# Optimization experiments

Measured on AMD Instinct MI355X. Metric: run time of the kernel, lower is better.

Reference implementation:

```python
import jax, jax.numpy as jnp
import numpy as np

N, E, G = 50000, 800000, 64        # nodes, edges, graphs in batch
IN, HID, OUT = 64, 128, 8


def gcn_conv(x, W, b, src, dst, num_nodes):
    """GCNConv: h = D^-1/2 (A+I) D^-1/2 (x W) + b, self-loops already in src/dst."""
    h = x @ W                                              # [N, out]
    deg = jax.ops.segment_sum(jnp.ones_like(dst, dtype=h.dtype), dst,
                              num_segments=num_nodes)      # [N]
    dinv = jax.lax.rsqrt(jnp.maximum(deg, 1.0))
    norm = dinv[src] * dinv[dst]                           # [E+N]
    msg = h[src] * norm[:, None]                           # gather + scale
    out = jax.ops.segment_sum(msg, dst, num_segments=num_nodes)
    return out + b


def global_mean_pool(x, batch, num_graphs):
    s = jax.ops.segment_sum(x, batch, num_segments=num_graphs)
    cnt = jax.ops.segment_sum(jnp.ones((x.shape[0],), x.dtype), batch,
                              num_segments=num_graphs)
    return s / jnp.maximum(cnt, 1.0)[:, None]


def setup_inputs() -> dict:
    key = jax.random.key(0)
    ks = jax.random.split(key, 11)
    def glorot(k, fi, fo):
        return jax.random.normal(k, (fi, fo), jnp.float32) * np.float32(1.0 / np.sqrt(fi))
    return {
        "x": jax.random.normal(ks[0], (N, IN), jnp.float32),
        "W1": glorot(ks[1], IN, HID),  "b1": jnp.zeros((HID,), jnp.float32),
        "W2": glorot(ks[2], HID, HID), "b2": jnp.zeros((HID,), jnp.float32),
        "W3": glorot(ks[3], HID, HID), "b3": jnp.zeros((HID,), jnp.float32),
        "Wh": glorot(ks[4], HID, OUT), "bh": jnp.zeros((OUT,), jnp.float32),
        "edge_index": jax.random.randint(ks[5], (2, E), 0, N),
        "batch": jnp.sort(jax.random.randint(ks[6], (N,), 0, G)),
    }


def reference(x, W1, b1, W2, b2, W3, b3, Wh, bh, edge_index, batch):
    loops = jnp.arange(N, dtype=edge_index.dtype)
    src = jnp.concatenate([edge_index[0], loops])          # add self-loops
    dst = jnp.concatenate([edge_index[1], loops])
    h = jax.nn.relu(gcn_conv(x, W1, b1, src, dst, N))
    h = jax.nn.relu(gcn_conv(h, W2, b2, src, dst, N))
    h = gcn_conv(h, W3, b3, src, dst, N)
    g = global_mean_pool(h, batch, G)                      # [G, HID]
    return g @ Wh + bh                                     # [G, OUT]
```

## Files before the change

### kernel.cpp

```cpp
#include <hip/hip_runtime.h>

typedef short bf8_t __attribute__((ext_vector_type(8)));
typedef float f32x4 __attribute__((ext_vector_type(4)));

__device__ inline unsigned short f2bf(float f) {
    unsigned u = __float_as_uint(f);
    return (unsigned short)((u + 0x7fff + ((u >> 16) & 1)) >> 16);
}


__global__ void deg_kernel(const int* __restrict__ dst, int* __restrict__ deg,
                           int* __restrict__ rank, int E) {
    int e = blockIdx.x * 256 + threadIdx.x;
    if (e < E) rank[e] = atomicAdd(&deg[dst[e]], 1);
}

__global__ void scan_blocksum(const int* __restrict__ deg, int* __restrict__ bsum,
                              float* __restrict__ dinv, int n) {
    int i = blockIdx.x * 256 + threadIdx.x;
    int d = (i < n) ? (deg[i] + 1) : 0;
    if (i < n) dinv[i] = rsqrtf((float)d);
    int v = d;
    for (int off = 32; off > 0; off >>= 1) v += __shfl_down(v, off, 64);
    __shared__ int ws[4];
    if ((threadIdx.x & 63) == 0) ws[threadIdx.x >> 6] = v;
    __syncthreads();
    if (threadIdx.x == 0) bsum[blockIdx.x] = ws[0] + ws[1] + ws[2] + ws[3];
}

__global__ void scan_offsets(const int* __restrict__ bsum, int* __restrict__ boff, int nblk) {
    __shared__ int buf[256];
    int tid = threadIdx.x;
    int v = (tid < nblk) ? bsum[tid] : 0;
    buf[tid] = v;
    __syncthreads();
    for (int off = 1; off < 256; off <<= 1) {
        int t = (tid >= off) ? buf[tid - off] : 0;
        __syncthreads();
        buf[tid] += t;
        __syncthreads();
    }
    if (tid < nblk) boff[tid] = buf[tid] - v;
}

__global__ void scan_rowptr(const int* __restrict__ deg, const int* __restrict__ boff,
                            int* __restrict__ row_ptr, int n) {
    __shared__ int buf[256];
    int tid = threadIdx.x;
    int i = blockIdx.x * 256 + tid;
    int v = (i < n) ? (deg[i] + 1) : 0;
    buf[tid] = v;
    __syncthreads();
    for (int off = 1; off < 256; off <<= 1) {
        int t = (tid >= off) ? buf[tid - off] : 0;
        __syncthreads();
        buf[tid] += t;
        __syncthreads();
    }
    int excl = buf[tid] - v + boff[blockIdx.x];
    if (i < n) row_ptr[i] = excl;
    if (i == n - 1) row_ptr[n] = excl + v;
}

__global__ void fill_kernel(const int* __restrict__ src, const int* __restrict__ dst,
                            const int* __restrict__ rank,
                            const int* __restrict__ row_ptr,
                            int* __restrict__ csr_src, int E, int n) {
    int e = blockIdx.x * 256 + threadIdx.x;
    if (e < E) {
        int s = src[e], d = dst[e];
        int pos = row_ptr[d] + 1 + rank[e];
        __builtin_nontemporal_store(s, &csr_src[pos]);
    } else if (e < E + n) {
        int s = e - E;
        __builtin_nontemporal_store(s, &csr_src[row_ptr[s]]);
    }
}

__global__ void x2bf_kernel(const float* __restrict__ x, const float* __restrict__ dinv,
                            unsigned* __restrict__ x16, int total8) {
    int i = blockIdx.x * 256 + threadIdx.x;
    if (i >= total8) return;
    float dn = dinv[i >> 3];
    const float4* x4 = (const float4*)x;
    float4 a = x4[i * 2], b = x4[i * 2 + 1];
    uint4 o;
    o.x = (unsigned)f2bf(a.x * dn) | ((unsigned)f2bf(a.y * dn) << 16);
    o.y = (unsigned)f2bf(a.z * dn) | ((unsigned)f2bf(a.w * dn) << 16);
    o.z = (unsigned)f2bf(b.x * dn) | ((unsigned)f2bf(b.y * dn) << 16);
    o.w = (unsigned)f2bf(b.z * dn) | ((unsigned)f2bf(b.w * dn) << 16);
    ((uint4*)x16)[i] = o;
}

__global__ void wt_all(const float* __restrict__ W1, const float* __restrict__ W2,
                       const float* __restrict__ W3,
                       unsigned short* __restrict__ Wt1, unsigned short* __restrict__ Wt2,
                       unsigned short* __restrict__ Wt3) {
    int i = blockIdx.x * 256 + threadIdx.x;
    if (i < 8192) {
        int nn = i / 64, k = i - nn * 64;
        Wt1[i] = f2bf(W1[k * 128 + nn]);
    } else if (i < 24576) {
        int j = i - 8192;
        int nn = j / 128, k = j - nn * 128;
        Wt2[j] = f2bf(W2[k * 128 + nn]);
    } else if (i < 40960) {
        int j = i - 24576;
        int nn = j / 128, k = j - nn * 128;
        Wt3[j] = f2bf(W3[k * 128 + nn]);
    }
}


__device__ inline void bf8_add(uint4 a, float* acc) {
#pragma unroll
    for (int j = 0; j < 4; ++j) {
        unsigned u = ((const unsigned*)&a)[j];
        acc[2 * j]     += __uint_as_float(u << 16);
        acc[2 * j + 1] += __uint_as_float(u & 0xffff0000u);
    }
}

__device__ inline uint4 pack_bf8(const float* v, float dn) {
    uint4 o;
    o.x = (unsigned)f2bf(v[0] * dn) | ((unsigned)f2bf(v[1] * dn) << 16);
    o.y = (unsigned)f2bf(v[2] * dn) | ((unsigned)f2bf(v[3] * dn) << 16);
    o.z = (unsigned)f2bf(v[4] * dn) | ((unsigned)f2bf(v[5] * dn) << 16);
    o.w = (unsigned)f2bf(v[6] * dn) | ((unsigned)f2bf(v[7] * dn) << 16);
    return o;
}

template<int K, bool RELU, bool BF16OUT>
__global__ __launch_bounds__(256) void agg_gemm(
        const unsigned short* __restrict__ in, const unsigned short* __restrict__ Wt16,
        const float* __restrict__ bias, void* __restrict__ outp,
        const int* __restrict__ row_ptr, const int* __restrict__ csr_src,
        const float* __restrict__ dinv, int n) {
    constexpr int KS = K / 32;
    __shared__ unsigned short As[16 * K];
    int w = threadIdx.x >> 6, lane = threadIdx.x & 63;
    int base = blockIdx.x * 16;
    int lr = lane & 15, lk = lane >> 4;

    bf8_t B[2][KS];
#pragma unroll
    for (int f = 0; f < 2; ++f) {
        int col = w * 32 + f * 16 + lr;
#pragma unroll
        for (int ks = 0; ks < KS; ++ks)
            B[f][ks] = *reinterpret_cast<const bf8_t*>(&Wt16[(size_t)col * K + ks * 32 + lk * 8]);
    }

    const uint4* in4 = (const uint4*)in;
    int g = lane >> 4;
    int row = w * 4 + g;
    int node = base + row;
    float acc[8] = {0.f, 0.f, 0.f, 0.f, 0.f, 0.f, 0.f, 0.f};

    if (K == 128) {
        int col = lane & 15;
        if (node < n) {
            int beg = row_ptr[node], end = row_ptr[node + 1];
            int i = beg;
            for (; i + 1 < end; i += 2) {
                int s0 = csr_src[i], s1 = csr_src[i + 1];
                uint4 a = in4[(size_t)s0 * 16 + col];
                uint4 b = in4[(size_t)s1 * 16 + col];
                bf8_add(a, acc);
                bf8_add(b, acc);
            }
            if (i < end) bf8_add(in4[(size_t)csr_src[i] * 16 + col], acc);
        }
        float dn = (node < n) ? dinv[node] : 0.f;
        int off = row * K + ((col * 8) ^ ((row & 7) << 3));
        *(uint4*)&As[off] = pack_bf8(acc, dn);
    } else {
        int sub = (lane >> 3) & 1;
        int col = lane & 7;
        if (node < n) {
            int beg = row_ptr[node], end = row_ptr[node + 1];
            int i = beg + sub;
            for (; i + 2 < end; i += 4) {
                int s0 = csr_src[i], s1 = csr_src[i + 2];
                uint4 a = in4[(size_t)s0 * 8 + col];
                uint4 b = in4[(size_t)s1 * 8 + col];
                bf8_add(a, acc);
                bf8_add(b, acc);
            }
            if (i < end) bf8_add(in4[(size_t)csr_src[i] * 8 + col], acc);
        }
#pragma unroll
        for (int j = 0; j < 8; ++j)
            acc[j] += __shfl_xor(acc[j], 8, 64);
        if (sub == 0) {
            float dn = (node < n) ? dinv[node] : 0.f;
            int off = row * K + ((col * 8) ^ ((row & 7) << 3));
            *(uint4*)&As[off] = pack_bf8(acc, dn);
        }
    }
    __syncthreads();

    f32x4 pacc[2] = {};
#pragma unroll
    for (int ks = 0; ks < KS; ++ks) {
        int off = lr * K + (((ks * 32) + lk * 8) ^ ((lr & 7) << 3));
        bf8_t a = *reinterpret_cast<const bf8_t*>(&As[off]);
#pragma unroll
        for (int f = 0; f < 2; ++f)
            pacc[f] = __builtin_amdgcn_mfma_f32_16x16x32_bf16(B[f][ks], a, pacc[f], 0, 0, 0);
    }

    int orow = base + lr;
    if (orow < n) {
        float dnx = BF16OUT ? dinv[orow] : 1.f;
#pragma unroll
        for (int f = 0; f < 2; ++f) {
            int c0 = w * 32 + f * 16 + lk * 4;
            float4 bv = *(const float4*)&bias[c0];
            float v0 = pacc[f][0] + bv.x, v1 = pacc[f][1] + bv.y;
            float v2 = pacc[f][2] + bv.z, v3 = pacc[f][3] + bv.w;
            if (RELU) {
                v0 = fmaxf(v0, 0.f); v1 = fmaxf(v1, 0.f);
                v2 = fmaxf(v2, 0.f); v3 = fmaxf(v3, 0.f);
            }
            if (BF16OUT) {
                uint2 o;
                o.x = (unsigned)f2bf(v0 * dnx) | ((unsigned)f2bf(v1 * dnx) << 16);
                o.y = (unsigned)f2bf(v2 * dnx) | ((unsigned)f2bf(v3 * dnx) << 16);
                *(uint2*)&((unsigned short*)outp)[(size_t)orow * 128 + c0] = o;
            } else {
                *(float4*)&((float*)outp)[(size_t)orow * 128 + c0] = make_float4(v0, v1, v2, v3);
            }
        }
    }
}


__global__ void gstart_bs(const int* __restrict__ batch, int* __restrict__ gstart,
                          int n, int G) {
    int g = blockIdx.x * blockDim.x + threadIdx.x;
    if (g > G) return;
    int lo = 0, hi = n;
    while (lo < hi) {
        int mid = (lo + hi) >> 1;
        if (batch[mid] < g) lo = mid + 1; else hi = mid;
    }
    gstart[g] = lo;
}

#define PSPLIT 16
__global__ __launch_bounds__(256) void pool_part(
        const float* __restrict__ h, const int* __restrict__ gstart,
        float* __restrict__ part) {
    int g = blockIdx.x >> 4, sp = blockIdx.x & (PSPLIT - 1);
    int tid = threadIdx.x;
    int c = tid & 127, rs = tid >> 7;
    int beg = gstart[g], end = gstart[g + 1];
    int len = end - beg;
    int chunk = (len + PSPLIT - 1) >> 4;
    int r0 = beg + sp * chunk;
    int r1 = min(r0 + chunk, end);
    float acc = 0.f;
    for (int r = r0 + rs; r < r1; r += 2)
        acc += h[(size_t)r * 128 + c];
    __shared__ float buf[256];
    buf[tid] = acc;
    __syncthreads();
    if (rs == 0)
        part[(size_t)blockIdx.x * 128 + c] = buf[c] + buf[c + 128];
}

__global__ __launch_bounds__(128) void pool_final(
        const float* __restrict__ part, const int* __restrict__ gstart,
        float* __restrict__ gout) {
    int g = blockIdx.x;
    int c = threadIdx.x;
    float acc = 0.f;
#pragma unroll
    for (int sp = 0; sp < PSPLIT; ++sp)
        acc += part[((size_t)g * PSPLIT + sp) * 128 + c];
    int cnt = gstart[g + 1] - gstart[g];
    gout[g * 128 + c] = acc / fmaxf((float)cnt, 1.f);
}

__global__ void head_kernel(const float* __restrict__ g, const float* __restrict__ Wh,
                            const float* __restrict__ bh, float* __restrict__ out, int G) {
    int tid = blockIdx.x * blockDim.x + threadIdx.x;
    if (tid >= G * 8) return;
    int gi = tid >> 3, o = tid & 7;
    float acc = bh[o];
    for (int k = 0; k < 128; ++k)
        acc = fmaf(g[gi * 128 + k], Wh[k * 8 + o], acc);
    out[tid] = acc;
}


extern "C" void kernel_launch(void* const* d_in, const int* in_sizes, int n_in,
                              void* d_out, int out_size, void* d_ws, size_t ws_size,
                              hipStream_t stream) {
    const float* x  = (const float*)d_in[0];
    const float* W1 = (const float*)d_in[1];
    const float* b1 = (const float*)d_in[2];
    const float* W2 = (const float*)d_in[3];
    const float* b2 = (const float*)d_in[4];
    const float* W3 = (const float*)d_in[5];
    const float* b3 = (const float*)d_in[6];
    const float* Wh = (const float*)d_in[7];
    const float* bh = (const float*)d_in[8];
    const int* edge_index = (const int*)d_in[9];
    const int* batch = (const int*)d_in[10];
    (void)n_in; (void)ws_size;

    const int N = in_sizes[10];
    const int E = in_sizes[9] / 2;
    const int G = out_size / 8;
    const int* esrc = edge_index;
    const int* edst = edge_index + E;

    size_t off = 0;
    auto take = [&](size_t bytes) {
        void* p = (char*)d_ws + off;
        off += (bytes + 255) & ~(size_t)255;
        return p;
    };
    int*   deg      = (int*)take((size_t)N * 4);
    float* dinv     = (float*)take((size_t)N * 4);
    int*   row_ptr  = (int*)take((size_t)(N + 1) * 4);
    int*   rank     = (int*)take((size_t)E * 4);
    int*   csr_src  = (int*)take((size_t)(E + N) * 4);
    int*   bsum     = (int*)take(256 * 4);
    int*   boff     = (int*)take(256 * 4);
    int*   gstart   = (int*)take((size_t)(G + 1) * 4);
    float* part     = (float*)take((size_t)G * PSPLIT * 128 * 4);
    float* gpool    = (float*)take((size_t)G * 128 * 4);
    unsigned short* x16  = (unsigned short*)take((size_t)N * 64 * 2);
    unsigned short* h16a = (unsigned short*)take((size_t)N * 128 * 2);
    unsigned short* h16b = (unsigned short*)take((size_t)N * 128 * 2);
    unsigned short* Wt1  = (unsigned short*)take((size_t)128 * 64 * 2);
    unsigned short* Wt2  = (unsigned short*)take((size_t)128 * 128 * 2);
    unsigned short* Wt3  = (unsigned short*)take((size_t)128 * 128 * 2);
    float* bufA     = (float*)take((size_t)N * 128 * 4);

    int nblk = (N + 255) / 256;
    int fgrid = (N + 15) / 16;

    hipMemsetAsync(deg, 0, (size_t)N * 4, stream);

    deg_kernel<<<(E + 255) / 256, 256, 0, stream>>>(edst, deg, rank, E);
    scan_blocksum<<<nblk, 256, 0, stream>>>(deg, bsum, dinv, N);
    scan_offsets<<<1, 256, 0, stream>>>(bsum, boff, nblk);
    scan_rowptr<<<nblk, 256, 0, stream>>>(deg, boff, row_ptr, N);
    fill_kernel<<<(E + N + 255) / 256, 256, 0, stream>>>(esrc, edst, rank, row_ptr, csr_src, E, N);
    x2bf_kernel<<<(N * 64 / 8 + 255) / 256, 256, 0, stream>>>(x, dinv, (unsigned*)x16, N * 64 / 8);
    wt_all<<<(40960 + 255) / 256, 256, 0, stream>>>(W1, W2, W3, Wt1, Wt2, Wt3);

    agg_gemm<64,  true,  true ><<<fgrid, 256, 0, stream>>>(x16,  Wt1, b1, h16a, row_ptr, csr_src, dinv, N);
    agg_gemm<128, true,  true ><<<fgrid, 256, 0, stream>>>(h16a, Wt2, b2, h16b, row_ptr, csr_src, dinv, N);
    agg_gemm<128, false, false><<<fgrid, 256, 0, stream>>>(h16b, Wt3, b3, bufA, row_ptr, csr_src, dinv, N);

    gstart_bs<<<1, 256, 0, stream>>>(batch, gstart, N, G);
    pool_part<<<G * PSPLIT, 256, 0, stream>>>(bufA, gstart, part);
    pool_final<<<G, 128, 0, stream>>>(part, gstart, gpool);
    head_kernel<<<(G * 8 + 255) / 256, 256, 0, stream>>>(gpool, Wh, bh, (float*)d_out, G);
}
```

Measured before the change: 226.9 us.

## Store CSR indices and ranks as 16-bit, prefetch neighbor indices, fuse gstart search

Narrows the per-edge rank and CSR source-index arrays from 32-bit to 16-bit, halving the bytes written in the fill step and read by each of the three aggregation kernels. The gather loops now software-prefetch the next pair of neighbor indices, and the CSR buffer is padded so those reads stay in bounds. The separate gstart binary-search kernel is removed, and the pooling kernels compute graph bounds inline, saving one launch. The 16-bit indices cannot represent node ids up to N=50000 that exceed 32767 as signed, though they fit as unsigned. Per-node degrees above 65535 would overflow the rank field.

```diff
diff --git a/kernel.cpp b/kernel.cpp
--- a/kernel.cpp
+++ b/kernel.cpp
@@ -2,17 +2,18 @@
 
 typedef short bf8_t __attribute__((ext_vector_type(8)));
 typedef float f32x4 __attribute__((ext_vector_type(4)));
-
-__device__ inline unsigned short f2bf(float f) {
+typedef unsigned short u16;
+
+__device__ inline u16 f2bf(float f) {
     unsigned u = __float_as_uint(f);
-    return (unsigned short)((u + 0x7fff + ((u >> 16) & 1)) >> 16);
+    return (u16)((u + 0x7fff + ((u >> 16) & 1)) >> 16);
 }
 
 
 __global__ void deg_kernel(const int* __restrict__ dst, int* __restrict__ deg,
-                           int* __restrict__ rank, int E) {
+                           u16* __restrict__ rank, int E) {
     int e = blockIdx.x * 256 + threadIdx.x;
-    if (e < E) rank[e] = atomicAdd(&deg[dst[e]], 1);
+    if (e < E) rank[e] = (u16)atomicAdd(&deg[dst[e]], 1);
 }
 
 __global__ void scan_blocksum(const int* __restrict__ deg, int* __restrict__ bsum,
@@ -63,17 +64,17 @@
 }
 
 __global__ void fill_kernel(const int* __restrict__ src, const int* __restrict__ dst,
-                            const int* __restrict__ rank,
+                            const u16* __restrict__ rank,
                             const int* __restrict__ row_ptr,
-                            int* __restrict__ csr_src, int E, int n) {
+                            u16* __restrict__ csr_src, int E, int n) {
     int e = blockIdx.x * 256 + threadIdx.x;
     if (e < E) {
         int s = src[e], d = dst[e];
-        int pos = row_ptr[d] + 1 + rank[e];
-        __builtin_nontemporal_store(s, &csr_src[pos]);
+        int pos = row_ptr[d] + 1 + (int)rank[e];
+        __builtin_nontemporal_store((u16)s, &csr_src[pos]);
     } else if (e < E + n) {
         int s = e - E;
-        __builtin_nontemporal_store(s, &csr_src[row_ptr[s]]);
+        __builtin_nontemporal_store((u16)s, &csr_src[row_ptr[s]]);
     }
 }
 
@@ -94,8 +95,8 @@
 
 __global__ void wt_all(const float* __restrict__ W1, const float* __restrict__ W2,
                        const float* __restrict__ W3,
-                       unsigned short* __restrict__ Wt1, unsigned short* __restrict__ Wt2,
-                       unsigned short* __restrict__ Wt3) {
+                       u16* __restrict__ Wt1, u16* __restrict__ Wt2,
+                       u16* __restrict__ Wt3) {
     int i = blockIdx.x * 256 + threadIdx.x;
     if (i < 8192) {
         int nn = i / 64, k = i - nn * 64;
@@ -132,12 +133,12 @@
 
 template<int K, bool RELU, bool BF16OUT>
 __global__ __launch_bounds__(256) void agg_gemm(
-        const unsigned short* __restrict__ in, const unsigned short* __restrict__ Wt16,
+        const u16* __restrict__ in, const u16* __restrict__ Wt16,
         const float* __restrict__ bias, void* __restrict__ outp,
-        const int* __restrict__ row_ptr, const int* __restrict__ csr_src,
+        const int* __restrict__ row_ptr, const u16* __restrict__ csr_src,
         const float* __restrict__ dinv, int n) {
     constexpr int KS = K / 32;
-    __shared__ unsigned short As[16 * K];
+    __shared__ u16 As[16 * K];
     int w = threadIdx.x >> 6, lane = threadIdx.x & 63;
     int base = blockIdx.x * 16;
     int lr = lane & 15, lk = lane >> 4;
@@ -162,14 +163,16 @@
         if (node < n) {
             int beg = row_ptr[node], end = row_ptr[node + 1];
             int i = beg;
+            int s0 = csr_src[i], s1 = csr_src[i + 1];
             for (; i + 1 < end; i += 2) {
-                int s0 = csr_src[i], s1 = csr_src[i + 1];
+                int t0 = csr_src[i + 2], t1 = csr_src[i + 3];
                 uint4 a = in4[(size_t)s0 * 16 + col];
                 uint4 b = in4[(size_t)s1 * 16 + col];
                 bf8_add(a, acc);
                 bf8_add(b, acc);
+                s0 = t0; s1 = t1;
             }
-            if (i < end) bf8_add(in4[(size_t)csr_src[i] * 16 + col], acc);
+            if (i < end) bf8_add(in4[(size_t)s0 * 16 + col], acc);
         }
         float dn = (node < n) ? dinv[node] : 0.f;
         int off = row * K + ((col * 8) ^ ((row & 7) << 3));
@@ -180,14 +183,16 @@
         if (node < n) {
             int beg = row_ptr[node], end = row_ptr[node + 1];
             int i = beg + sub;
+            int s0 = csr_src[i], s1 = csr_src[i + 2];
             for (; i + 2 < end; i += 4) {
-                int s0 = csr_src[i], s1 = csr_src[i + 2];
+                int t0 = csr_src[i + 4], t1 = csr_src[i + 6];
                 uint4 a = in4[(size_t)s0 * 8 + col];
                 uint4 b = in4[(size_t)s1 * 8 + col];
                 bf8_add(a, acc);
                 bf8_add(b, acc);
+                s0 = t0; s1 = t1;
             }
-            if (i < end) bf8_add(in4[(size_t)csr_src[i] * 8 + col], acc);
+            if (i < end) bf8_add(in4[(size_t)s0 * 8 + col], acc);
         }
 #pragma unroll
         for (int j = 0; j < 8; ++j)
@@ -227,7 +232,7 @@
                 uint2 o;
                 o.x = (unsigned)f2bf(v0 * dnx) | ((unsigned)f2bf(v1 * dnx) << 16);
                 o.y = (unsigned)f2bf(v2 * dnx) | ((unsigned)f2bf(v3 * dnx) << 16);
-                *(uint2*)&((unsigned short*)outp)[(size_t)orow * 128 + c0] = o;
+                *(uint2*)&((u16*)outp)[(size_t)orow * 128 + c0] = o;
             } else {
                 *(float4*)&((float*)outp)[(size_t)orow * 128 + c0] = make_float4(v0, v1, v2, v3);
             }
@@ -236,26 +241,23 @@
 }
 
 
-__global__ void gstart_bs(const int* __restrict__ batch, int* __restrict__ gstart,
-                          int n, int G) {
-    int g = blockIdx.x * blockDim.x + threadIdx.x;
-    if (g > G) return;
+__device__ inline int lbound(const int* __restrict__ batch, int n, int g) {
     int lo = 0, hi = n;
     while (lo < hi) {
         int mid = (lo + hi) >> 1;
         if (batch[mid] < g) lo = mid + 1; else hi = mid;
     }
-    gstart[g] = lo;
+    return lo;
 }
 
 #define PSPLIT 16
 __global__ __launch_bounds__(256) void pool_part(
-        const float* __restrict__ h, const int* __restrict__ gstart,
-        float* __restrict__ part) {
+        const float* __restrict__ h, const int* __restrict__ batch,
+        float* __restrict__ part, int n) {
     int g = blockIdx.x >> 4, sp = blockIdx.x & (PSPLIT - 1);
     int tid = threadIdx.x;
     int c = tid & 127, rs = tid >> 7;
-    int beg = gstart[g], end = gstart[g + 1];
+    int beg = lbound(batch, n, g), end = lbound(batch, n, g + 1);
     int len = end - beg;
     int chunk = (len + PSPLIT - 1) >> 4;
     int r0 = beg + sp * chunk;
@@ -271,15 +273,15 @@
 }
 
 __global__ __launch_bounds__(128) void pool_final(
-        const float* __restrict__ part, const int* __restrict__ gstart,
-        float* __restrict__ gout) {
+        const float* __restrict__ part, const int* __restrict__ batch,
+        float* __restrict__ gout, int n) {
     int g = blockIdx.x;
     int c = threadIdx.x;
     float acc = 0.f;
 #pragma unroll
     for (int sp = 0; sp < PSPLIT; ++sp)
         acc += part[((size_t)g * PSPLIT + sp) * 128 + c];
-    int cnt = gstart[g + 1] - gstart[g];
+    int cnt = lbound(batch, n, g + 1) - lbound(batch, n, g);
     gout[g * 128 + c] = acc / fmaxf((float)cnt, 1.f);
 }
 
@@ -326,19 +328,18 @@
     int*   deg      = (int*)take((size_t)N * 4);
     float* dinv     = (float*)take((size_t)N * 4);
     int*   row_ptr  = (int*)take((size_t)(N + 1) * 4);
-    int*   rank     = (int*)take((size_t)E * 4);
-    int*   csr_src  = (int*)take((size_t)(E + N) * 4);
+    u16*   rank     = (u16*)take((size_t)E * 2);
+    u16*   csr_src  = (u16*)take((size_t)(E + N + 64) * 2);
     int*   bsum     = (int*)take(256 * 4);
     int*   boff     = (int*)take(256 * 4);
-    int*   gstart   = (int*)take((size_t)(G + 1) * 4);
     float* part     = (float*)take((size_t)G * PSPLIT * 128 * 4);
     float* gpool    = (float*)take((size_t)G * 128 * 4);
-    unsigned short* x16  = (unsigned short*)take((size_t)N * 64 * 2);
-    unsigned short* h16a = (unsigned short*)take((size_t)N * 128 * 2);
-    unsigned short* h16b = (unsigned short*)take((size_t)N * 128 * 2);
-    unsigned short* Wt1  = (unsigned short*)take((size_t)128 * 64 * 2);
-    unsigned short* Wt2  = (unsigned short*)take((size_t)128 * 128 * 2);
-    unsigned short* Wt3  = (unsigned short*)take((size_t)128 * 128 * 2);
+    u16*   x16      = (u16*)take((size_t)N * 64 * 2);
+    u16*   h16a     = (u16*)take((size_t)N * 128 * 2);
+    u16*   h16b     = (u16*)take((size_t)N * 128 * 2);
+    u16*   Wt1      = (u16*)take((size_t)128 * 64 * 2);
+    u16*   Wt2      = (u16*)take((size_t)128 * 128 * 2);
+    u16*   Wt3      = (u16*)take((size_t)128 * 128 * 2);
     float* bufA     = (float*)take((size_t)N * 128 * 4);
 
     int nblk = (N + 255) / 256;
@@ -358,8 +359,7 @@
     agg_gemm<128, true,  true ><<<fgrid, 256, 0, stream>>>(h16a, Wt2, b2, h16b, row_ptr, csr_src, dinv, N);
     agg_gemm<128, false, false><<<fgrid, 256, 0, stream>>>(h16b, Wt3, b3, bufA, row_ptr, csr_src, dinv, N);
 
-    gstart_bs<<<1, 256, 0, stream>>>(batch, gstart, N, G);
-    pool_part<<<G * PSPLIT, 256, 0, stream>>>(bufA, gstart, part);
-    pool_final<<<G, 128, 0, stream>>>(part, gstart, gpool);
+    pool_part<<<G * PSPLIT, 256, 0, stream>>>(bufA, batch, part, N);
+    pool_final<<<G, 128, 0, stream>>>(part, batch, gpool, N);
     head_kernel<<<(G * 8 + 255) / 256, 256, 0, stream>>>(gpool, Wh, bh, (float*)d_out, G);
 }
```

New measurement: 224.5 us. About the same (-1.0%).
